# Kernel optimization log

Hardware: AMD Instinct MI355X
Metric: run time of the kernel (lower is better)

## Reference

```python
import jax, jax.numpy as jnp
import numpy as np

N = 100000
E = 1600000
D = 64
EPS = 1e-5


def setup_inputs() -> dict:
    key = jax.random.key(0)
    ks = jax.random.split(key, 16)
    x = jax.random.normal(ks[0], (N, D), dtype=jnp.float32)
    edge_index = jax.random.randint(ks[1], (2, E), 0, N, dtype=jnp.int64)
    s = 1.0 / np.sqrt(D)
    params = {
        'W1': jax.random.uniform(ks[2], (D, D), jnp.float32, -s, s),
        'b1': jnp.zeros((D,), jnp.float32),
        'g1': jnp.ones((D,), jnp.float32),
        'be1': jnp.zeros((D,), jnp.float32),
        'W2': jax.random.uniform(ks[3], (D, D), jnp.float32, -s, s),
        'b2': jnp.zeros((D,), jnp.float32),
        'g2': jnp.ones((D,), jnp.float32),
        'be2': jnp.zeros((D,), jnp.float32),
        'W3': jax.random.uniform(ks[4], (D, D), jnp.float32, -s, s),
        'b3': jnp.zeros((D,), jnp.float32),
    }
    return {'x': x, 'edge_index': edge_index, **params}


def _gcn_norm(edge_index):
    # add self-loops, symmetric normalization (PyG GCNConv default)
    loop = jnp.arange(N, dtype=edge_index.dtype)
    src = jnp.concatenate([edge_index[0], loop])  # [E+N]
    dst = jnp.concatenate([edge_index[1], loop])
    deg = jax.ops.segment_sum(jnp.ones_like(src, dtype=jnp.float32), dst, num_segments=N)
    dinv = jnp.where(deg > 0, jax.lax.rsqrt(deg), 0.0)
    norm = dinv[src] * dinv[dst]  # [E+N]
    return src, dst, norm


def _gcn_conv(x, src, dst, norm, W, b):
    h = x @ W                        # [N, D] transform first (PyG order)
    msg = h[src] * norm[:, None]     # gather + scale  [E+N, D]
    out = jax.ops.segment_sum(msg, dst, num_segments=N)  # scatter-add
    return out + b


def _bn(x, g, b):
    # BatchNorm1d over nodes, batch statistics (training-mode math)
    m = jnp.mean(x, axis=0)
    v = jnp.var(x, axis=0)
    return g * (x - m) * jax.lax.rsqrt(v + EPS) + b


def reference(x, edge_index, W1, b1, g1, be1, W2, b2, g2, be2, W3, b3):
    src, dst, norm = _gcn_norm(edge_index)
    h = _gcn_conv(x, src, dst, norm, W1, b1)
    h = jax.nn.relu(_bn(h, g1, be1))
    h = _gcn_conv(h, src, dst, norm, W2, b2)
    h = jax.nn.relu(_bn(h, g2, be2))
    h = _gcn_conv(h, src, dst, norm, W3, b3)
    return h
```

## Files before the change

kernel.cpp:

```cpp
#include <hip/hip_runtime.h>
#include <hip/hip_bf16.h>


#define FD 64
#define EPSF 1e-5f

#define NBUCK 256
#define BSHIFT 9
#define BWID 512
#define SLOTS 28
#define P1_EDGES 4096

typedef __attribute__((ext_vector_type(8))) short bf16x8;
typedef __attribute__((ext_vector_type(4))) float f32x4;

__device__ __forceinline__ float bf2f(ushort u) {
  return __uint_as_float((unsigned)u << 16);
}
__device__ __forceinline__ ushort f2bf_bits(float f) {
  __hip_bfloat16 h = __float2bfloat16(f);
  return *(ushort*)&h;
}

__global__ __launch_bounds__(256) void init_kernel(const int* __restrict__ ei,
                                                   int* __restrict__ flag,
                                                   int* __restrict__ bhist,
                                                   float* __restrict__ stats1,
                                                   float* __restrict__ stats2) {
  int t = threadIdx.x;
  bhist[t] = 0;
  if (t < 128) {
    stats1[t] = 0.f;
    stats2[t] = 0.f;
  }
  if (t < 64) {
    int v = ei[2 * t + 1];
    unsigned long long nz = __ballot(v != 0);
    if (t == 0) *flag = (nz == 0ull) ? 1 : 0;
  }
}

__global__ __launch_bounds__(256) void hist_kernel(const int* __restrict__ ei, int E,
                                                   const int* __restrict__ flag,
                                                   int* __restrict__ bhist) {
  __shared__ int h[NBUCK];
  const int tid = threadIdx.x;
  h[tid] = 0;
  __syncthreads();
  const int is64 = *flag;
  const int base = blockIdx.x * P1_EDGES;
#pragma unroll 1
  for (int k = 0; k < P1_EDGES / 256; ++k) {
    int e = base + k * 256 + tid;
    if (e < E) {
      int d = is64 ? ei[2 * (E + e)] : ei[E + e];
      atomicAdd(&h[d >> BSHIFT], 1);
    }
  }
  __syncthreads();
  if (h[tid]) atomicAdd(&bhist[tid], h[tid]);
}

__global__ __launch_bounds__(256) void bscan_kernel(const int* __restrict__ bhist,
                                                    int* __restrict__ bbase,
                                                    int* __restrict__ bcur) {
  __shared__ int lds[NBUCK];
  int t = threadIdx.x;
  int v = bhist[t];
  lds[t] = v;
  __syncthreads();
  for (int off = 1; off < NBUCK; off <<= 1) {
    int tv = (t >= off) ? lds[t - off] : 0;
    __syncthreads();
    lds[t] += tv;
    __syncthreads();
  }
  int ex = lds[t] - v;
  bbase[t] = ex;
  bcur[t] = ex;
}

__global__ __launch_bounds__(256) void fill1_kernel(const int* __restrict__ ei, int E,
                                                    const int* __restrict__ flag,
                                                    int* __restrict__ bcur,
                                                    int2* __restrict__ stage) {
  __shared__ int2 sbuf[NBUCK][SLOTS];
  __shared__ int scnt[NBUCK];
  __shared__ int sbase[NBUCK];
  const int tid = threadIdx.x;
  scnt[tid] = 0;
  __syncthreads();
  const int is64 = *flag;
  const int base = blockIdx.x * P1_EDGES;
#pragma unroll 1
  for (int k = 0; k < P1_EDGES / 256; ++k) {
    int e = base + k * 256 + tid;
    if (e < E) {
      int s = is64 ? ei[2 * e] : ei[e];
      int d = is64 ? ei[2 * (E + e)] : ei[E + e];
      int b = d >> BSHIFT;
      int pos = atomicAdd(&scnt[b], 1);
      if (pos < SLOTS) {
        sbuf[b][pos] = make_int2(s, d);
      } else {
        stage[atomicAdd(&bcur[b], 1)] = make_int2(s, d);
      }
    }
  }
  __syncthreads();
  {
    int c = scnt[tid];
    if (c > SLOTS) c = SLOTS;
    scnt[tid] = c;
    sbase[tid] = c ? atomicAdd(&bcur[tid], c) : 0;
  }
  __syncthreads();
  for (int idx = tid; idx < NBUCK * SLOTS; idx += 256) {
    int b = idx / SLOTS, sl = idx - b * SLOTS;
    if (sl < scnt[b]) stage[sbase[b] + sl] = sbuf[b][sl];
  }
}

__global__ __launch_bounds__(256) void degcount_kernel(const int2* __restrict__ stage,
                                                       const int* __restrict__ bbase,
                                                       const int* __restrict__ bcur,
                                                       int* __restrict__ deg,
                                                       float* __restrict__ dinv, int N) {
  __shared__ int h[BWID];
  const int b = blockIdx.x;
  const int tid = threadIdx.x;
  for (int i = tid; i < BWID; i += 256) h[i] = 0;
  __syncthreads();
  const int lo = bbase[b], hi = bcur[b];
  for (int i = lo + tid; i < hi; i += 256)
    atomicAdd(&h[stage[i].y - (b << BSHIFT)], 1);
  __syncthreads();
  const int n0 = b << BSHIFT;
  for (int i = tid; i < BWID; i += 256) {
    int node = n0 + i;
    if (node < N) {
      int d = h[i];
      deg[node] = d;
      dinv[node] = rsqrtf((float)(d + 1));
    }
  }
}

__global__ __launch_bounds__(1024) void scan1_kernel(const int* __restrict__ deg,
                                                     int* __restrict__ rowptr,
                                                     int* __restrict__ partial, int N) {
  __shared__ int lds[1024];
  int i = blockIdx.x * 1024 + threadIdx.x;
  int v = (i < N) ? deg[i] : 0;
  lds[threadIdx.x] = v;
  __syncthreads();
  for (int off = 1; off < 1024; off <<= 1) {
    int t = (threadIdx.x >= (unsigned)off) ? lds[threadIdx.x - off] : 0;
    __syncthreads();
    lds[threadIdx.x] += t;
    __syncthreads();
  }
  if (i < N) rowptr[i + 1] = lds[threadIdx.x];
  if (threadIdx.x == 1023) partial[blockIdx.x] = lds[1023];
}

__global__ __launch_bounds__(128) void scan2_kernel(int* __restrict__ partial, int B) {
  __shared__ int lds[128];
  int t = threadIdx.x;
  int v = (t < B) ? partial[t] : 0;
  lds[t] = v;
  __syncthreads();
  for (int off = 1; off < 128; off <<= 1) {
    int tv = (t >= off) ? lds[t - off] : 0;
    __syncthreads();
    lds[t] += tv;
    __syncthreads();
  }
  if (t < B) partial[t] = lds[t] - v;
}

__global__ __launch_bounds__(1024) void scan3_kernel(const int* __restrict__ deg,
                                                     int* __restrict__ rowptr,
                                                     const int* __restrict__ partial,
                                                     int* __restrict__ cursor, int N) {
  int i = blockIdx.x * 1024 + threadIdx.x;
  if (i < N) {
    int r = rowptr[i + 1] + partial[blockIdx.x];
    rowptr[i + 1] = r;
    cursor[i] = r - deg[i];
    if (i == 0) rowptr[0] = 0;
  }
}

__global__ __launch_bounds__(256) void fill2_kernel(const int2* __restrict__ stage,
                                                    const int* __restrict__ bbase,
                                                    const int* __restrict__ bcur,
                                                    int* __restrict__ cursor,
                                                    const float* __restrict__ dinv,
                                                    int2* __restrict__ colw) {
  const int b = blockIdx.x >> 1;
  const int half = blockIdx.x & 1;
  const int lo = bbase[b];
  const int hi = bcur[b];
  for (int i = lo + half * 256 + threadIdx.x; i < hi; i += 512) {
    int2 sd = stage[i];
    int slot = atomicAdd(&cursor[sd.y], 1);
    colw[slot] = make_int2(sd.x, __float_as_int(dinv[sd.x] * dinv[sd.y]));
  }
}

__global__ __launch_bounds__(256) void deg_atomic_kernel(const int* __restrict__ ei, int E,
                                                         const int* __restrict__ flag,
                                                         int* __restrict__ deg) {
  int e = blockIdx.x * 256 + threadIdx.x;
  if (e >= E) return;
  const int is64 = *flag;
  int d = is64 ? ei[2 * (E + e)] : ei[E + e];
  atomicAdd(&deg[d], 1);
}
__global__ __launch_bounds__(256) void dinv_kernel(const int* __restrict__ deg,
                                                   float* __restrict__ dinv, int N) {
  int i = blockIdx.x * 256 + threadIdx.x;
  if (i < N) dinv[i] = rsqrtf((float)(deg[i] + 1));
}
__global__ __launch_bounds__(256) void fill_direct_kernel(const int* __restrict__ ei, int E,
                                                          const int* __restrict__ flag,
                                                          const float* __restrict__ dinv,
                                                          int* __restrict__ cursor,
                                                          int2* __restrict__ colw) {
  int e = blockIdx.x * 256 + threadIdx.x;
  if (e >= E) return;
  const int is64 = *flag;
  int s = is64 ? ei[2 * e] : ei[e];
  int d = is64 ? ei[2 * (E + e)] : ei[E + e];
  int slot = atomicAdd(&cursor[d], 1);
  colw[slot] = make_int2(s, __float_as_int(dinv[s] * dinv[d]));
}

__global__ __launch_bounds__(256) void cast_kernel(const float* __restrict__ in,
                                                   ushort* __restrict__ out, int total) {
  int i = (blockIdx.x * 256 + threadIdx.x) * 4;
  if (i >= total) return;
  float4 v = *(const float4*)(in + i);
  ushort4 o;
  o.x = f2bf_bits(v.x);
  o.y = f2bf_bits(v.y);
  o.z = f2bf_bits(v.z);
  o.w = f2bf_bits(v.w);
  *(ushort4*)(out + i) = o;
}

template <bool BN>
__global__ __launch_bounds__(256) void agg_kernel(const ushort* __restrict__ H,
                                                  const int* __restrict__ rowptr,
                                                  const int2* __restrict__ colw,
                                                  const float* __restrict__ dinv,
                                                  const float* __restrict__ stats,
                                                  const float* __restrict__ g,
                                                  const float* __restrict__ be,
                                                  ushort* __restrict__ out, int N) {
  const int lane = threadIdx.x & 63;
  const int wid = threadIdx.x >> 6;
  const int grp = lane >> 4;
  const int fl = lane & 15;
  const int dst = (blockIdx.x * 4 + wid) * 4 + grp;
  const bool live = dst < N;
  const int dc = live ? dst : N - 1;

  float a[4], cc[4];
  if (BN) {
    const float invN = 1.0f / (float)N;
#pragma unroll
    for (int j = 0; j < 4; ++j) {
      int f = fl * 4 + j;
      float m = stats[f] * invN;
      float v = stats[64 + f] * invN - m * m;
      float r = rsqrtf(v + EPSF);
      a[j] = g[f] * r;
      cc[j] = be[f] - m * a[j];
    }
  }

  const int e0 = rowptr[dc];
  const int e1 = live ? rowptr[dc + 1] : e0;
  const float di = dinv[dc];

  float acc[4][4];
#pragma unroll
  for (int u = 0; u < 4; ++u)
#pragma unroll
    for (int j = 0; j < 4; ++j) acc[u][j] = 0.f;

  {
    uint2 uv = *(const uint2*)(H + (size_t)dc * FD + fl * 4);
    float h0 = __uint_as_float(uv.x << 16);
    float h1 = __uint_as_float(uv.x & 0xffff0000u);
    float h2 = __uint_as_float(uv.y << 16);
    float h3 = __uint_as_float(uv.y & 0xffff0000u);
    if (BN) {
      h0 = fmaxf(fmaf(a[0], h0, cc[0]), 0.f);
      h1 = fmaxf(fmaf(a[1], h1, cc[1]), 0.f);
      h2 = fmaxf(fmaf(a[2], h2, cc[2]), 0.f);
      h3 = fmaxf(fmaf(a[3], h3, cc[3]), 0.f);
    }
    const float dsq = di * di;
    acc[0][0] = dsq * h0;
    acc[0][1] = dsq * h1;
    acc[0][2] = dsq * h2;
    acc[0][3] = dsq * h3;
  }

  for (int base = e0; __any(base < e1); base += 4) {
#pragma unroll
    for (int u = 0; u < 4; ++u) {
      const int ee = base + u;
      const bool valid = ee < e1;
      const int idx = valid ? ee : 0;
      const int2 cw = colw[idx];
      const float w = valid ? __int_as_float(cw.y) : 0.f;
      uint2 uv = *(const uint2*)(H + (size_t)cw.x * FD + fl * 4);
      float h0 = __uint_as_float(uv.x << 16);
      float h1 = __uint_as_float(uv.x & 0xffff0000u);
      float h2 = __uint_as_float(uv.y << 16);
      float h3 = __uint_as_float(uv.y & 0xffff0000u);
      if (BN) {
        h0 = fmaxf(fmaf(a[0], h0, cc[0]), 0.f);
        h1 = fmaxf(fmaf(a[1], h1, cc[1]), 0.f);
        h2 = fmaxf(fmaf(a[2], h2, cc[2]), 0.f);
        h3 = fmaxf(fmaf(a[3], h3, cc[3]), 0.f);
      }
      acc[u][0] = fmaf(w, h0, acc[u][0]);
      acc[u][1] = fmaf(w, h1, acc[u][1]);
      acc[u][2] = fmaf(w, h2, acc[u][2]);
      acc[u][3] = fmaf(w, h3, acc[u][3]);
    }
  }

  if (live) {
    ushort4 o;
    o.x = f2bf_bits((acc[0][0] + acc[1][0]) + (acc[2][0] + acc[3][0]));
    o.y = f2bf_bits((acc[0][1] + acc[1][1]) + (acc[2][1] + acc[3][1]));
    o.z = f2bf_bits((acc[0][2] + acc[1][2]) + (acc[2][2] + acc[3][2]));
    o.w = f2bf_bits((acc[0][3] + acc[1][3]) + (acc[2][3] + acc[3][3]));
    *(ushort4*)(out + (size_t)dst * FD + fl * 4) = o;
  }
}

template <bool BF16OUT>
__global__ __launch_bounds__(256) void gemm_mfma_kernel(const ushort* __restrict__ A,
                                                        const float* __restrict__ W,
                                                        const float* __restrict__ bias,
                                                        ushort* __restrict__ outb,
                                                        float* __restrict__ outf,
                                                        float* __restrict__ stats, int N) {
  const int lane = threadIdx.x & 63;
  const int wid = threadIdx.x >> 6;
  const int lo = lane & 15;
  const int hi = lane >> 4;

  __shared__ float sred[128];
  if (BF16OUT) {
    if (threadIdx.x < 128) sred[threadIdx.x] = 0.f;
    __syncthreads();
  }

  bf16x8 bfrag[2][4];
#pragma unroll
  for (int kk = 0; kk < 2; ++kk)
#pragma unroll
    for (int nt = 0; nt < 4; ++nt)
#pragma unroll
      for (int j = 0; j < 8; ++j) {
        int k = kk * 32 + hi * 8 + j;
        bfrag[kk][nt][j] = (short)f2bf_bits(W[k * FD + nt * 16 + lo]);
      }

  float bl[4];
#pragma unroll
  for (int nt = 0; nt < 4; ++nt) bl[nt] = bias[nt * 16 + lo];

  float s1[4] = {0.f, 0.f, 0.f, 0.f};
  float s2[4] = {0.f, 0.f, 0.f, 0.f};

  const int TILES = (N + 15) / 16;
  const int stride = gridDim.x * 4;
  for (int tile = blockIdx.x * 4 + wid; tile < TILES; tile += stride) {
    const int row0 = tile * 16;
    const int ar = min(row0 + lo, N - 1);
    const ushort* ap = A + (size_t)ar * FD + hi * 8;
    bf16x8 a0 = *(const bf16x8*)ap;
    bf16x8 a1 = *(const bf16x8*)(ap + 32);

    f32x4 acc[4] = {{0.f, 0.f, 0.f, 0.f},
                    {0.f, 0.f, 0.f, 0.f},
                    {0.f, 0.f, 0.f, 0.f},
                    {0.f, 0.f, 0.f, 0.f}};
#pragma unroll
    for (int nt = 0; nt < 4; ++nt) {
      acc[nt] = __builtin_amdgcn_mfma_f32_16x16x32_bf16(a0, bfrag[0][nt], acc[nt], 0, 0, 0);
      acc[nt] = __builtin_amdgcn_mfma_f32_16x16x32_bf16(a1, bfrag[1][nt], acc[nt], 0, 0, 0);
    }

#pragma unroll
    for (int nt = 0; nt < 4; ++nt) {
#pragma unroll
      for (int r = 0; r < 4; ++r) {
        int row = row0 + hi * 4 + r;
        if (row < N) {
          float o = acc[nt][r] + bl[nt];
          if (BF16OUT) {
            outb[(size_t)row * FD + nt * 16 + lo] = f2bf_bits(o);
            s1[nt] += o;
            s2[nt] += o * o;
          } else {
            outf[(size_t)row * FD + nt * 16 + lo] = o;
          }
        }
      }
    }
  }

  if (BF16OUT) {
#pragma unroll
    for (int nt = 0; nt < 4; ++nt) {
      atomicAdd(&sred[nt * 16 + lo], s1[nt]);
      atomicAdd(&sred[64 + nt * 16 + lo], s2[nt]);
    }
    __syncthreads();
    if (threadIdx.x < 128) atomicAdd(&stats[threadIdx.x], sred[threadIdx.x]);
  }
}

extern "C" void kernel_launch(void* const* d_in, const int* in_sizes, int n_in,
                              void* d_out, int out_size, void* d_ws, size_t ws_size,
                              hipStream_t stream) {
  const float* x = (const float*)d_in[0];
  const int* ei = (const int*)d_in[1];
  const float* W1 = (const float*)d_in[2];
  const float* b1 = (const float*)d_in[3];
  const float* g1 = (const float*)d_in[4];
  const float* be1 = (const float*)d_in[5];
  const float* W2 = (const float*)d_in[6];
  const float* b2 = (const float*)d_in[7];
  const float* g2 = (const float*)d_in[8];
  const float* be2 = (const float*)d_in[9];
  const float* W3 = (const float*)d_in[10];
  const float* b3 = (const float*)d_in[11];

  const int N = in_sizes[0] / FD;
  const int E = in_sizes[1] / 2;
  const int nB = (N + BWID - 1) >> BSHIFT;

  char* p = (char*)d_ws;
  auto alloc = [&](size_t bytes) {
    char* r = p;
    p += (bytes + 255) & ~(size_t)255;
    return r;
  };
  int* flag = (int*)alloc(4);
  float* stats1 = (float*)alloc(128 * 4);
  float* stats2 = (float*)alloc(128 * 4);
  int* partial = (int*)alloc(128 * 4);
  int* bhist = (int*)alloc(NBUCK * 4);
  int* bbase = (int*)alloc(NBUCK * 4);
  int* bcur = (int*)alloc(NBUCK * 4);
  int* deg = (int*)alloc((size_t)N * 4);
  float* dinv = (float*)alloc((size_t)N * 4);
  int* rowptr = (int*)alloc((size_t)(N + 1) * 4);
  int* cursor = (int*)alloc((size_t)N * 4);
  int2* colw = (int2*)alloc((size_t)E * 8);
  ushort* T0 = (ushort*)alloc((size_t)N * FD * 2);
  ushort* T1 = (ushort*)alloc((size_t)N * FD * 2);
  size_t base_need = (size_t)(p - (char*)d_ws);
  int2* stage = (int2*)alloc((size_t)E * 8);
  size_t full_need = (size_t)(p - (char*)d_ws);
  const bool two_phase =
      ((ws_size == 0) || (ws_size >= full_need)) && (N <= NBUCK * BWID);
  (void)base_need;

  const int NB = (N + 1023) / 1024;
  const int EB = (E + P1_EDGES - 1) / P1_EDGES;

  init_kernel<<<1, 256, 0, stream>>>(ei, flag, bhist, stats1, stats2);

  if (two_phase) {
    hist_kernel<<<EB, 256, 0, stream>>>(ei, E, flag, bhist);
    bscan_kernel<<<1, NBUCK, 0, stream>>>(bhist, bbase, bcur);
    fill1_kernel<<<EB, 256, 0, stream>>>(ei, E, flag, bcur, stage);
    degcount_kernel<<<nB, 256, 0, stream>>>(stage, bbase, bcur, deg, dinv, N);
    scan1_kernel<<<NB, 1024, 0, stream>>>(deg, rowptr, partial, N);
    scan2_kernel<<<1, 128, 0, stream>>>(partial, NB);
    scan3_kernel<<<NB, 1024, 0, stream>>>(deg, rowptr, partial, cursor, N);
    fill2_kernel<<<2 * nB, 256, 0, stream>>>(stage, bbase, bcur, cursor, dinv, colw);
  } else {
    hipMemsetAsync(deg, 0, (size_t)N * 4, stream);
    deg_atomic_kernel<<<(E + 255) / 256, 256, 0, stream>>>(ei, E, flag, deg);
    dinv_kernel<<<(N + 255) / 256, 256, 0, stream>>>(deg, dinv, N);
    scan1_kernel<<<NB, 1024, 0, stream>>>(deg, rowptr, partial, N);
    scan2_kernel<<<1, 128, 0, stream>>>(partial, NB);
    scan3_kernel<<<NB, 1024, 0, stream>>>(deg, rowptr, partial, cursor, N);
    fill_direct_kernel<<<(E + 255) / 256, 256, 0, stream>>>(ei, E, flag, dinv, cursor,
                                                            colw);
  }

  const int aggGrid = (N + 15) / 16;
  const int castGrid = (N * FD / 4 + 255) / 256;
  const int TILES = (N + 15) / 16;
  const int gemmGrid = (TILES + 15) / 16;

  cast_kernel<<<castGrid, 256, 0, stream>>>(x, T0, N * FD);
  agg_kernel<false><<<aggGrid, 256, 0, stream>>>(T0, rowptr, colw, dinv, nullptr, nullptr,
                                                 nullptr, T1, N);
  gemm_mfma_kernel<true><<<gemmGrid, 256, 0, stream>>>(T1, W1, b1, T0, nullptr, stats1, N);

  agg_kernel<true><<<aggGrid, 256, 0, stream>>>(T0, rowptr, colw, dinv, stats1, g1, be1,
                                                T1, N);
  gemm_mfma_kernel<true><<<gemmGrid, 256, 0, stream>>>(T1, W2, b2, T0, nullptr, stats2, N);

  agg_kernel<true><<<aggGrid, 256, 0, stream>>>(T0, rowptr, colw, dinv, stats2, g2, be2,
                                                T1, N);
  gemm_mfma_kernel<false><<<gemmGrid, 256, 0, stream>>>(T1, W3, b3, nullptr,
                                                        (float*)d_out, nullptr, N);
}
```

Before: 317.3 us.

## Fuse degree count with bucket-local scan; split BN-ReLU out; widen aggregation loads

Replaces degcount plus the three-kernel global scan with one degscan kernel. Each bucket block builds a local histogram and an exclusive scan, then offsets it by the bucket base to write rowptr, cursor and dinv directly. BN+ReLU is moved out of the aggregation gather into a standalone elementwise pass over the node features, so the per-edge gather no longer recomputes the affine and ReLU. The aggregation kernel now loads 16-byte rows (8 bf16 per lane) and splits edges across two half-groups combined with a shuffle, in exchange for an extra full read and write of the feature matrix per BN layer.

```diff
diff --git a/kernel.cpp b/kernel.cpp
--- a/kernel.cpp
+++ b/kernel.cpp
@@ -14,12 +14,12 @@
 typedef __attribute__((ext_vector_type(8))) short bf16x8;
 typedef __attribute__((ext_vector_type(4))) float f32x4;
 
-__device__ __forceinline__ float bf2f(ushort u) {
-  return __uint_as_float((unsigned)u << 16);
-}
 __device__ __forceinline__ ushort f2bf_bits(float f) {
   __hip_bfloat16 h = __float2bfloat16(f);
   return *(ushort*)&h;
+}
+__device__ __forceinline__ unsigned packbf(float lo, float hi) {
+  return (unsigned)f2bf_bits(lo) | ((unsigned)f2bf_bits(hi) << 16);
 }
 
 __global__ __launch_bounds__(256) void init_kernel(const int* __restrict__ ei,
@@ -121,75 +121,50 @@
   }
 }
 
-__global__ __launch_bounds__(256) void degcount_kernel(const int2* __restrict__ stage,
-                                                       const int* __restrict__ bbase,
-                                                       const int* __restrict__ bcur,
-                                                       int* __restrict__ deg,
-                                                       float* __restrict__ dinv, int N) {
+__global__ __launch_bounds__(256) void degscan_kernel(const int2* __restrict__ stage,
+                                                      const int* __restrict__ bbase,
+                                                      const int* __restrict__ bcur,
+                                                      int* __restrict__ rowptr,
+                                                      int* __restrict__ cursor,
+                                                      float* __restrict__ dinv,
+                                                      int N, int nB) {
   __shared__ int h[BWID];
+  __shared__ int ps[256];
   const int b = blockIdx.x;
   const int tid = threadIdx.x;
-  for (int i = tid; i < BWID; i += 256) h[i] = 0;
+  h[tid] = 0;
+  h[tid + 256] = 0;
   __syncthreads();
   const int lo = bbase[b], hi = bcur[b];
   for (int i = lo + tid; i < hi; i += 256)
     atomicAdd(&h[stage[i].y - (b << BSHIFT)], 1);
   __syncthreads();
+  const int a0 = h[2 * tid], a1 = h[2 * tid + 1];
+  ps[tid] = a0 + a1;
+  __syncthreads();
+  for (int off = 1; off < 256; off <<= 1) {
+    int v = (tid >= off) ? ps[tid - off] : 0;
+    __syncthreads();
+    ps[tid] += v;
+    __syncthreads();
+  }
+  const int excl = ps[tid] - (a0 + a1);
   const int n0 = b << BSHIFT;
-  for (int i = tid; i < BWID; i += 256) {
-    int node = n0 + i;
-    if (node < N) {
-      int d = h[i];
-      deg[node] = d;
-      dinv[node] = rsqrtf((float)(d + 1));
-    }
-  }
-}
-
-__global__ __launch_bounds__(1024) void scan1_kernel(const int* __restrict__ deg,
-                                                     int* __restrict__ rowptr,
-                                                     int* __restrict__ partial, int N) {
-  __shared__ int lds[1024];
-  int i = blockIdx.x * 1024 + threadIdx.x;
-  int v = (i < N) ? deg[i] : 0;
-  lds[threadIdx.x] = v;
-  __syncthreads();
-  for (int off = 1; off < 1024; off <<= 1) {
-    int t = (threadIdx.x >= (unsigned)off) ? lds[threadIdx.x - off] : 0;
-    __syncthreads();
-    lds[threadIdx.x] += t;
-    __syncthreads();
-  }
-  if (i < N) rowptr[i + 1] = lds[threadIdx.x];
-  if (threadIdx.x == 1023) partial[blockIdx.x] = lds[1023];
-}
-
-__global__ __launch_bounds__(128) void scan2_kernel(int* __restrict__ partial, int B) {
-  __shared__ int lds[128];
-  int t = threadIdx.x;
-  int v = (t < B) ? partial[t] : 0;
-  lds[t] = v;
-  __syncthreads();
-  for (int off = 1; off < 128; off <<= 1) {
-    int tv = (t >= off) ? lds[t - off] : 0;
-    __syncthreads();
-    lds[t] += tv;
-    __syncthreads();
-  }
-  if (t < B) partial[t] = lds[t] - v;
-}
-
-__global__ __launch_bounds__(1024) void scan3_kernel(const int* __restrict__ deg,
-                                                     int* __restrict__ rowptr,
-                                                     const int* __restrict__ partial,
-                                                     int* __restrict__ cursor, int N) {
-  int i = blockIdx.x * 1024 + threadIdx.x;
-  if (i < N) {
-    int r = rowptr[i + 1] + partial[blockIdx.x];
-    rowptr[i + 1] = r;
-    cursor[i] = r - deg[i];
-    if (i == 0) rowptr[0] = 0;
-  }
+  const int na = n0 + 2 * tid;
+  const int nb2 = na + 1;
+  if (na < N) {
+    int r = lo + excl;
+    rowptr[na] = r;
+    cursor[na] = r;
+    dinv[na] = rsqrtf((float)(a0 + 1));
+  }
+  if (nb2 < N) {
+    int r = lo + excl + a0;
+    rowptr[nb2] = r;
+    cursor[nb2] = r;
+    dinv[nb2] = rsqrtf((float)(a1 + 1));
+  }
+  if (b == nB - 1 && tid == 255) rowptr[N] = lo + ps[255];
 }
 
 __global__ __launch_bounds__(256) void fill2_kernel(const int2* __restrict__ stage,
@@ -223,6 +198,49 @@
   int i = blockIdx.x * 256 + threadIdx.x;
   if (i < N) dinv[i] = rsqrtf((float)(deg[i] + 1));
 }
+__global__ __launch_bounds__(1024) void scan1_kernel(const int* __restrict__ deg,
+                                                     int* __restrict__ rowptr,
+                                                     int* __restrict__ partial, int N) {
+  __shared__ int lds[1024];
+  int i = blockIdx.x * 1024 + threadIdx.x;
+  int v = (i < N) ? deg[i] : 0;
+  lds[threadIdx.x] = v;
+  __syncthreads();
+  for (int off = 1; off < 1024; off <<= 1) {
+    int t = (threadIdx.x >= (unsigned)off) ? lds[threadIdx.x - off] : 0;
+    __syncthreads();
+    lds[threadIdx.x] += t;
+    __syncthreads();
+  }
+  if (i < N) rowptr[i + 1] = lds[threadIdx.x];
+  if (threadIdx.x == 1023) partial[blockIdx.x] = lds[1023];
+}
+__global__ __launch_bounds__(128) void scan2_kernel(int* __restrict__ partial, int B) {
+  __shared__ int lds[128];
+  int t = threadIdx.x;
+  int v = (t < B) ? partial[t] : 0;
+  lds[t] = v;
+  __syncthreads();
+  for (int off = 1; off < 128; off <<= 1) {
+    int tv = (t >= off) ? lds[t - off] : 0;
+    __syncthreads();
+    lds[t] += tv;
+    __syncthreads();
+  }
+  if (t < B) partial[t] = lds[t] - v;
+}
+__global__ __launch_bounds__(1024) void scan3_kernel(const int* __restrict__ deg,
+                                                     int* __restrict__ rowptr,
+                                                     const int* __restrict__ partial,
+                                                     int* __restrict__ cursor, int N) {
+  int i = blockIdx.x * 1024 + threadIdx.x;
+  if (i < N) {
+    int r = rowptr[i + 1] + partial[blockIdx.x];
+    rowptr[i + 1] = r;
+    cursor[i] = r - deg[i];
+    if (i == 0) rowptr[0] = 0;
+  }
+}
 __global__ __launch_bounds__(256) void fill_direct_kernel(const int* __restrict__ ei, int E,
                                                           const int* __restrict__ flag,
                                                           const float* __restrict__ dinv,
@@ -250,99 +268,119 @@
   *(ushort4*)(out + i) = o;
 }
 
-template <bool BN>
+__global__ __launch_bounds__(256) void bnrelu_kernel(ushort* __restrict__ T,
+                                                     const float* __restrict__ stats,
+                                                     const float* __restrict__ g,
+                                                     const float* __restrict__ be,
+                                                     int N) {
+  __shared__ float sa[FD], sc[FD];
+  if (threadIdx.x < FD) {
+    const float invN = 1.0f / (float)N;
+    float m = stats[threadIdx.x] * invN;
+    float v = stats[FD + threadIdx.x] * invN - m * m;
+    float r = rsqrtf(v + EPSF);
+    float a = g[threadIdx.x] * r;
+    sa[threadIdx.x] = a;
+    sc[threadIdx.x] = be[threadIdx.x] - m * a;
+  }
+  __syncthreads();
+  const int idx = (blockIdx.x * 256 + threadIdx.x) * 8;
+  if (idx >= N * FD) return;
+  const int f0 = idx & (FD - 1);
+  uint4 v = *(const uint4*)(T + idx);
+  float h0 = __uint_as_float(v.x << 16);
+  float h1 = __uint_as_float(v.x & 0xffff0000u);
+  float h2 = __uint_as_float(v.y << 16);
+  float h3 = __uint_as_float(v.y & 0xffff0000u);
+  float h4 = __uint_as_float(v.z << 16);
+  float h5 = __uint_as_float(v.z & 0xffff0000u);
+  float h6 = __uint_as_float(v.w << 16);
+  float h7 = __uint_as_float(v.w & 0xffff0000u);
+  h0 = fmaxf(fmaf(sa[f0 + 0], h0, sc[f0 + 0]), 0.f);
+  h1 = fmaxf(fmaf(sa[f0 + 1], h1, sc[f0 + 1]), 0.f);
+  h2 = fmaxf(fmaf(sa[f0 + 2], h2, sc[f0 + 2]), 0.f);
+  h3 = fmaxf(fmaf(sa[f0 + 3], h3, sc[f0 + 3]), 0.f);
+  h4 = fmaxf(fmaf(sa[f0 + 4], h4, sc[f0 + 4]), 0.f);
+  h5 = fmaxf(fmaf(sa[f0 + 5], h5, sc[f0 + 5]), 0.f);
+  h6 = fmaxf(fmaf(sa[f0 + 6], h6, sc[f0 + 6]), 0.f);
+  h7 = fmaxf(fmaf(sa[f0 + 7], h7, sc[f0 + 7]), 0.f);
+  uint4 o;
+  o.x = packbf(h0, h1);
+  o.y = packbf(h2, h3);
+  o.z = packbf(h4, h5);
+  o.w = packbf(h6, h7);
+  *(uint4*)(T + idx) = o;
+}
+
 __global__ __launch_bounds__(256) void agg_kernel(const ushort* __restrict__ H,
                                                   const int* __restrict__ rowptr,
                                                   const int2* __restrict__ colw,
                                                   const float* __restrict__ dinv,
-                                                  const float* __restrict__ stats,
-                                                  const float* __restrict__ g,
-                                                  const float* __restrict__ be,
                                                   ushort* __restrict__ out, int N) {
   const int lane = threadIdx.x & 63;
   const int wid = threadIdx.x >> 6;
   const int grp = lane >> 4;
-  const int fl = lane & 15;
+  const int sg = (lane >> 3) & 1;
+  const int fl8 = lane & 7;
   const int dst = (blockIdx.x * 4 + wid) * 4 + grp;
   const bool live = dst < N;
   const int dc = live ? dst : N - 1;
 
-  float a[4], cc[4];
-  if (BN) {
-    const float invN = 1.0f / (float)N;
-#pragma unroll
-    for (int j = 0; j < 4; ++j) {
-      int f = fl * 4 + j;
-      float m = stats[f] * invN;
-      float v = stats[64 + f] * invN - m * m;
-      float r = rsqrtf(v + EPSF);
-      a[j] = g[f] * r;
-      cc[j] = be[f] - m * a[j];
-    }
-  }
-
   const int e0 = rowptr[dc];
   const int e1 = live ? rowptr[dc + 1] : e0;
-  const float di = dinv[dc];
-
-  float acc[4][4];
+
+  float acc[4][8];
 #pragma unroll
   for (int u = 0; u < 4; ++u)
 #pragma unroll
-    for (int j = 0; j < 4; ++j) acc[u][j] = 0.f;
-
-  {
-    uint2 uv = *(const uint2*)(H + (size_t)dc * FD + fl * 4);
-    float h0 = __uint_as_float(uv.x << 16);
-    float h1 = __uint_as_float(uv.x & 0xffff0000u);
-    float h2 = __uint_as_float(uv.y << 16);
-    float h3 = __uint_as_float(uv.y & 0xffff0000u);
-    if (BN) {
-      h0 = fmaxf(fmaf(a[0], h0, cc[0]), 0.f);
-      h1 = fmaxf(fmaf(a[1], h1, cc[1]), 0.f);
-      h2 = fmaxf(fmaf(a[2], h2, cc[2]), 0.f);
-      h3 = fmaxf(fmaf(a[3], h3, cc[3]), 0.f);
-    }
-    const float dsq = di * di;
-    acc[0][0] = dsq * h0;
-    acc[0][1] = dsq * h1;
-    acc[0][2] = dsq * h2;
-    acc[0][3] = dsq * h3;
-  }
-
-  for (int base = e0; __any(base < e1); base += 4) {
+    for (int j = 0; j < 8; ++j) acc[u][j] = 0.f;
+
+  for (int base = e0; __any(base < e1); base += 8) {
 #pragma unroll
     for (int u = 0; u < 4; ++u) {
-      const int ee = base + u;
+      const int ee = base + 2 * u + sg;
       const bool valid = ee < e1;
       const int idx = valid ? ee : 0;
       const int2 cw = colw[idx];
       const float w = valid ? __int_as_float(cw.y) : 0.f;
-      uint2 uv = *(const uint2*)(H + (size_t)cw.x * FD + fl * 4);
-      float h0 = __uint_as_float(uv.x << 16);
-      float h1 = __uint_as_float(uv.x & 0xffff0000u);
-      float h2 = __uint_as_float(uv.y << 16);
-      float h3 = __uint_as_float(uv.y & 0xffff0000u);
-      if (BN) {
-        h0 = fmaxf(fmaf(a[0], h0, cc[0]), 0.f);
-        h1 = fmaxf(fmaf(a[1], h1, cc[1]), 0.f);
-        h2 = fmaxf(fmaf(a[2], h2, cc[2]), 0.f);
-        h3 = fmaxf(fmaf(a[3], h3, cc[3]), 0.f);
-      }
-      acc[u][0] = fmaf(w, h0, acc[u][0]);
-      acc[u][1] = fmaf(w, h1, acc[u][1]);
-      acc[u][2] = fmaf(w, h2, acc[u][2]);
-      acc[u][3] = fmaf(w, h3, acc[u][3]);
+      const uint4 uv = *(const uint4*)(H + (size_t)cw.x * FD + fl8 * 8);
+      acc[u][0] = fmaf(w, __uint_as_float(uv.x << 16), acc[u][0]);
+      acc[u][1] = fmaf(w, __uint_as_float(uv.x & 0xffff0000u), acc[u][1]);
+      acc[u][2] = fmaf(w, __uint_as_float(uv.y << 16), acc[u][2]);
+      acc[u][3] = fmaf(w, __uint_as_float(uv.y & 0xffff0000u), acc[u][3]);
+      acc[u][4] = fmaf(w, __uint_as_float(uv.z << 16), acc[u][4]);
+      acc[u][5] = fmaf(w, __uint_as_float(uv.z & 0xffff0000u), acc[u][5]);
+      acc[u][6] = fmaf(w, __uint_as_float(uv.w << 16), acc[u][6]);
+      acc[u][7] = fmaf(w, __uint_as_float(uv.w & 0xffff0000u), acc[u][7]);
     }
   }
 
-  if (live) {
-    ushort4 o;
-    o.x = f2bf_bits((acc[0][0] + acc[1][0]) + (acc[2][0] + acc[3][0]));
-    o.y = f2bf_bits((acc[0][1] + acc[1][1]) + (acc[2][1] + acc[3][1]));
-    o.z = f2bf_bits((acc[0][2] + acc[1][2]) + (acc[2][2] + acc[3][2]));
-    o.w = f2bf_bits((acc[0][3] + acc[1][3]) + (acc[2][3] + acc[3][3]));
-    *(ushort4*)(out + (size_t)dst * FD + fl * 4) = o;
+  float r[8];
+#pragma unroll
+  for (int j = 0; j < 8; ++j)
+    r[j] = (acc[0][j] + acc[1][j]) + (acc[2][j] + acc[3][j]);
+#pragma unroll
+  for (int j = 0; j < 8; ++j) r[j] += __shfl_xor(r[j], 8);
+
+  const float di = dinv[dc];
+  const float dsq = di * di;
+  const uint4 sv = *(const uint4*)(H + (size_t)dc * FD + fl8 * 8);
+  r[0] = fmaf(dsq, __uint_as_float(sv.x << 16), r[0]);
+  r[1] = fmaf(dsq, __uint_as_float(sv.x & 0xffff0000u), r[1]);
+  r[2] = fmaf(dsq, __uint_as_float(sv.y << 16), r[2]);
+  r[3] = fmaf(dsq, __uint_as_float(sv.y & 0xffff0000u), r[3]);
+  r[4] = fmaf(dsq, __uint_as_float(sv.z << 16), r[4]);
+  r[5] = fmaf(dsq, __uint_as_float(sv.z & 0xffff0000u), r[5]);
+  r[6] = fmaf(dsq, __uint_as_float(sv.w << 16), r[6]);
+  r[7] = fmaf(dsq, __uint_as_float(sv.w & 0xffff0000u), r[7]);
+
+  if (live && sg == 0) {
+    uint4 o;
+    o.x = packbf(r[0], r[1]);
+    o.y = packbf(r[2], r[3]);
+    o.z = packbf(r[4], r[5]);
+    o.w = packbf(r[6], r[7]);
+    *(uint4*)(out + (size_t)dst * FD + fl8 * 8) = o;
   }
 }
 
@@ -487,10 +525,8 @@
     hist_kernel<<<EB, 256, 0, stream>>>(ei, E, flag, bhist);
     bscan_kernel<<<1, NBUCK, 0, stream>>>(bhist, bbase, bcur);
     fill1_kernel<<<EB, 256, 0, stream>>>(ei, E, flag, bcur, stage);
-    degcount_kernel<<<nB, 256, 0, stream>>>(stage, bbase, bcur, deg, dinv, N);
-    scan1_kernel<<<NB, 1024, 0, stream>>>(deg, rowptr, partial, N);
-    scan2_kernel<<<1, 128, 0, stream>>>(partial, NB);
-    scan3_kernel<<<NB, 1024, 0, stream>>>(deg, rowptr, partial, cursor, N);
+    degscan_kernel<<<nB, 256, 0, stream>>>(stage, bbase, bcur, rowptr, cursor, dinv, N,
+                                           nB);
     fill2_kernel<<<2 * nB, 256, 0, stream>>>(stage, bbase, bcur, cursor, dinv, colw);
   } else {
     hipMemsetAsync(deg, 0, (size_t)N * 4, stream);
@@ -505,20 +541,20 @@
 
   const int aggGrid = (N + 15) / 16;
   const int castGrid = (N * FD / 4 + 255) / 256;
+  const int bnGrid = (N * FD / 8 + 255) / 256;
   const int TILES = (N + 15) / 16;
   const int gemmGrid = (TILES + 15) / 16;
 
   cast_kernel<<<castGrid, 256, 0, stream>>>(x, T0, N * FD);
-  agg_kernel<false><<<aggGrid, 256, 0, stream>>>(T0, rowptr, colw, dinv, nullptr, nullptr,
-                                                 nullptr, T1, N);
+  agg_kernel<<<aggGrid, 256, 0, stream>>>(T0, rowptr, colw, dinv, T1, N);
   gemm_mfma_kernel<true><<<gemmGrid, 256, 0, stream>>>(T1, W1, b1, T0, nullptr, stats1, N);
 
-  agg_kernel<true><<<aggGrid, 256, 0, stream>>>(T0, rowptr, colw, dinv, stats1, g1, be1,
-                                                T1, N);
+  bnrelu_kernel<<<bnGrid, 256, 0, stream>>>(T0, stats1, g1, be1, N);
+  agg_kernel<<<aggGrid, 256, 0, stream>>>(T0, rowptr, colw, dinv, T1, N);
   gemm_mfma_kernel<true><<<gemmGrid, 256, 0, stream>>>(T1, W2, b2, T0, nullptr, stats2, N);
 
-  agg_kernel<true><<<aggGrid, 256, 0, stream>>>(T0, rowptr, colw, dinv, stats2, g2, be2,
-                                                T1, N);
+  bnrelu_kernel<<<bnGrid, 256, 0, stream>>>(T0, stats2, g2, be2, N);
+  agg_kernel<<<aggGrid, 256, 0, stream>>>(T0, rowptr, colw, dinv, T1, N);
   gemm_mfma_kernel<false><<<gemmGrid, 256, 0, stream>>>(T1, W3, b3, nullptr,
                                                         (float*)d_out, nullptr, N);
 }
```

Result: faster. 308.9 us (-2.6%).
